# Kernel optimization log

Hardware: AMD Instinct MI355X
Metric: run time of the kernel (lower is better)

The kernel has to match this reference:

```python
import jax, jax.numpy as jnp
import numpy as np

N, L, D, A, K = 8192, 200, 64, 5, 4

def setup_inputs() -> dict:
    key = jax.random.key(0)
    k1, k2, k3, k4, k5, k6 = jax.random.split(key, 6)
    return {
        "behavior_embs": jax.random.normal(k1, (N, L, D), dtype=jnp.float32),
        "pratical_seq_len": jax.random.randint(k2, (N,), 1, L + 1),
        "W1_w": jax.random.normal(k3, (A, D), dtype=jnp.float32) * (1.0 / np.sqrt(D)),
        "W1_b": jax.random.normal(k4, (A,), dtype=jnp.float32) * 0.01,
        "W2_w": jax.random.normal(k5, (K, A), dtype=jnp.float32) * (1.0 / np.sqrt(A)),
        "W2_b": jax.random.normal(k6, (K,), dtype=jnp.float32) * 0.01,
    }

def reference(behavior_embs, pratical_seq_len, W1_w, W1_b, W2_w, W2_b):
    n, l, d = behavior_embs.shape
    valid = jnp.arange(l) < pratical_seq_len[:, None]          # [N, L] bool
    h = behavior_embs
    # tiny MLP attention scores: [N, L, K]
    s = jnp.tanh(jnp.einsum('nld,ad->nla', h, W1_w) + W1_b)
    s = jnp.einsum('nla,ka->nlk', s, W2_w) + W2_b
    s = jnp.where(valid[:, :, None], s, -jnp.inf)              # mask invalid positions
    s = jnp.swapaxes(s, -1, -2)                                # [N, K, L]
    # global-max-shifted softmax over seq dim (matches torch: subtract tensor-wide max)
    e = jnp.exp(s - jnp.max(s))                                # masked -> exp(-inf)=0
    denom = jnp.sum(e, axis=-1, keepdims=True)
    p = e / jnp.where(denom == 0, 1.0, denom)                  # all-masked rows -> 0 (torch nan->0)
    # weighted sum over sequence: [N, K, D]
    return jnp.einsum('nkl,nld->nkd', p, h)
```

## Files before the change

kernel.cpp:

```cpp
#include <hip/hip_runtime.h>
#include <math.h>


#define LL 200
#define DD 64
#define AA 5
#define KK 4
#define RPW 50
#define WU2 832
#define FREG (WU2 * 2)

__device__ __forceinline__ unsigned bf16_rne(float f) {
    unsigned u = __float_as_uint(f);
    return (u + 0x7FFFu + ((u >> 16) & 1u)) >> 16;
}
__device__ __forceinline__ unsigned pk2(float lo, float hi) {
    return bf16_rne(lo) | (bf16_rne(hi) << 16);
}
__device__ __forceinline__ float lo16(unsigned u) { return __uint_as_float(u << 16); }
__device__ __forceinline__ float hi16(unsigned u) { return __uint_as_float(u & 0xFFFF0000u); }

__device__ __forceinline__ float fast_tanh(float x) {
    float e = __expf(2.f * x);
    return 1.f - 2.f * __builtin_amdgcn_rcpf(e + 1.f);
}

__global__ __launch_bounds__(256, 5)
void mie_fused(const float* __restrict__ h_g,
               const int*   __restrict__ slen_g,
               const float* __restrict__ W1w,
               const float* __restrict__ W1b,
               const float* __restrict__ W2w,
               const float* __restrict__ W2b,
               float*       __restrict__ out)
{
    __shared__ uint2  hbuf[4 * WU2];
    __shared__ float4 p4s[4][52];
    __shared__ float  den_s[4][4][KK];

    const int n    = blockIdx.x;
    const int t    = threadIdx.x;
    const int w    = t >> 6;
    const int lane = t & 63;
    const int slen = slen_g[n];

    const int nrows = min(max(slen - w * RPW, 0), RPW);
    uint2* hbw     = &hbuf[w * WU2];
    float* fregion = (float*)hbw;

    if (nrows == 0) {
        float4 z = {0.f, 0.f, 0.f, 0.f};
        #pragma unroll
        for (int q = 0; q < 4; ++q)
            *(float4*)&fregion[q * 256 + lane * 4] = z;
        if (lane < 4) *(float4*)&den_s[w][lane][0] = z;
    } else {
        const int nf4  = slen * 16;
        const float4* hn4 = (const float4*)(h_g + (size_t)n * (LL * DD));
        const int base = w * RPW * 16;
        const int jmax = (nrows + 3) >> 2;

        for (int j0 = 0; j0 < jmax; j0 += 4) {
            float4 rn[4];
            #pragma unroll
            for (int u = 0; u < 4; ++u) {
                int i = (j0 + u) * 64 + lane;
                rn[u] = hn4[min(base + i, nf4 - 1)];
            }
            #pragma unroll
            for (int u = 0; u < 4; ++u) {
                int j = j0 + u;
                if (j < jmax) {
                    int i = j * 64 + lane;
                    int r = i >> 4, c = i & 15;
                    hbw[r * 16 + (c ^ (r & 15))] =
                        make_uint2(pk2(rn[u].x, rn[u].y), pk2(rn[u].z, rn[u].w));
                }
            }
        }

        float Bk[KK];
        #pragma unroll
        for (int k = 0; k < KK; ++k) {
            float b = fabsf(W2b[k]);
            #pragma unroll
            for (int a = 0; a < AA; ++a) b += fabsf(W2w[k * AA + a]);
            Bk[k] = b;
        }

        asm volatile("s_waitcnt lgkmcnt(0)" ::: "memory");

        const float4* W14 = (const float4*)W1w;
        const int rl = min(lane, nrows - 1);
        float a0 = W1b[0], a1 = W1b[1], a2 = W1b[2], a3 = W1b[3], a4 = W1b[4];
        #pragma unroll
        for (int i = 0; i < 16; ++i) {
            uint2 q = hbw[rl * 16 + (i ^ (rl & 15))];
            float hx = lo16(q.x), hy = hi16(q.x), hz = lo16(q.y), hw = hi16(q.y);
            float4 w0 = W14[0*16+i], w1 = W14[1*16+i], w2 = W14[2*16+i],
                   w3 = W14[3*16+i], w4 = W14[4*16+i];
            a0 = fmaf(hx, w0.x, fmaf(hy, w0.y, fmaf(hz, w0.z, fmaf(hw, w0.w, a0))));
            a1 = fmaf(hx, w1.x, fmaf(hy, w1.y, fmaf(hz, w1.z, fmaf(hw, w1.w, a1))));
            a2 = fmaf(hx, w2.x, fmaf(hy, w2.y, fmaf(hz, w2.z, fmaf(hw, w2.w, a2))));
            a3 = fmaf(hx, w3.x, fmaf(hy, w3.y, fmaf(hz, w3.z, fmaf(hw, w3.w, a3))));
            a4 = fmaf(hx, w4.x, fmaf(hy, w4.y, fmaf(hz, w4.z, fmaf(hw, w4.w, a4))));
        }
        const bool vrow = lane < nrows;
        const float t0 = fast_tanh(a0), t1 = fast_tanh(a1), t2 = fast_tanh(a2),
                    t3 = fast_tanh(a3), t4 = fast_tanh(a4);
        float e[KK];
        #pragma unroll
        for (int k = 0; k < KK; ++k) {
            float s = W2b[k];
            s = fmaf(t0, W2w[k*AA+0], s);
            s = fmaf(t1, W2w[k*AA+1], s);
            s = fmaf(t2, W2w[k*AA+2], s);
            s = fmaf(t3, W2w[k*AA+3], s);
            s = fmaf(t4, W2w[k*AA+4], s);
            e[k] = vrow ? __expf(s - Bk[k]) : 0.f;
        }
        if (lane < 52)
            p4s[w][lane] = make_float4(e[0], e[1], e[2], e[3]);

        asm volatile("s_waitcnt lgkmcnt(0)" ::: "memory");

        const int rq = lane >> 4, dc = lane & 15;
        float4 acc0 = {0,0,0,0}, acc1 = {0,0,0,0}, acc2 = {0,0,0,0}, acc3 = {0,0,0,0};
        float dn0 = 0.f, dn1 = 0.f, dn2 = 0.f, dn3 = 0.f;
        for (int g = 0; g < jmax; ++g) {
            const int row = g * 4 + rq;
            uint2 q = hbw[row * 16 + (dc ^ (row & 15))];
            float hx = lo16(q.x), hy = hi16(q.x), hz = lo16(q.y), hw = hi16(q.y);
            float4 pv = p4s[w][row];
            acc0.x = fmaf(pv.x, hx, acc0.x); acc0.y = fmaf(pv.x, hy, acc0.y);
            acc0.z = fmaf(pv.x, hz, acc0.z); acc0.w = fmaf(pv.x, hw, acc0.w);
            acc1.x = fmaf(pv.y, hx, acc1.x); acc1.y = fmaf(pv.y, hy, acc1.y);
            acc1.z = fmaf(pv.y, hz, acc1.z); acc1.w = fmaf(pv.y, hw, acc1.w);
            acc2.x = fmaf(pv.z, hx, acc2.x); acc2.y = fmaf(pv.z, hy, acc2.y);
            acc2.z = fmaf(pv.z, hz, acc2.z); acc2.w = fmaf(pv.z, hw, acc2.w);
            acc3.x = fmaf(pv.w, hx, acc3.x); acc3.y = fmaf(pv.w, hy, acc3.y);
            acc3.z = fmaf(pv.w, hz, acc3.z); acc3.w = fmaf(pv.w, hw, acc3.w);
            dn0 += pv.x; dn1 += pv.y; dn2 += pv.z; dn3 += pv.w;
        }

        *(float4*)&fregion[rq * 256 + 0 * 64 + dc * 4] = acc0;
        *(float4*)&fregion[rq * 256 + 1 * 64 + dc * 4] = acc1;
        *(float4*)&fregion[rq * 256 + 2 * 64 + dc * 4] = acc2;
        *(float4*)&fregion[rq * 256 + 3 * 64 + dc * 4] = acc3;
        if (dc == 0)
            *(float4*)&den_s[w][rq][0] = make_float4(dn0, dn1, dn2, dn3);
    }

    __syncthreads();

    {
        const float* fb = (const float*)hbuf;
        float s = 0.f;
        #pragma unroll
        for (int i = 0; i < 16; ++i)
            s += fb[(i >> 2) * FREG + (i & 3) * 256 + t];
        const int k = t >> 6;
        float den = 0.f;
        #pragma unroll
        for (int i = 0; i < 16; ++i)
            den += den_s[i >> 2][i & 3][k];
        out[(size_t)n * (KK * DD) + t] = s / den;
    }
}

extern "C" void kernel_launch(void* const* d_in, const int* in_sizes, int n_in,
                              void* d_out, int out_size, void* d_ws, size_t ws_size,
                              hipStream_t stream) {
    const float* h_g  = (const float*)d_in[0];
    const int*   slen = (const int*)  d_in[1];
    const float* W1w  = (const float*)d_in[2];
    const float* W1b  = (const float*)d_in[3];
    const float* W2w  = (const float*)d_in[4];
    const float* W2b  = (const float*)d_in[5];
    float*       outp = (float*)d_out;

    const int N = in_sizes[1];

    mie_fused<<<dim3(N), dim3(256), 0, stream>>>(h_g, slen, W1w, W1b, W2w, W2b, outp);
}
```

Measured before the change: 58.84 us.

## Convert to persistent blocks with atomic work queue and register prefetch

Replaces the one-block-per-row launch with a persistent grid of up to 1024 blocks that take rows from an atomic counter. Each wave prefetches the next row's 13 float4s per lane into registers while it computes on the current row held in LDS. The goal is to overlap global loads with compute and cut per-block launch and tail overhead. In exchange it adds a memset before every launch, an atomic per row, larger register use (occupancy hint lowered from 5 to 4), and relies on the workspace counter.

```diff
diff --git a/kernel.cpp b/kernel.cpp
--- a/kernel.cpp
+++ b/kernel.cpp
@@ -25,146 +25,177 @@
     return 1.f - 2.f * __builtin_amdgcn_rcpf(e + 1.f);
 }
 
-__global__ __launch_bounds__(256, 5)
+__global__ __launch_bounds__(256, 4)
 void mie_fused(const float* __restrict__ h_g,
                const int*   __restrict__ slen_g,
                const float* __restrict__ W1w,
                const float* __restrict__ W1b,
                const float* __restrict__ W2w,
                const float* __restrict__ W2b,
-               float*       __restrict__ out)
+               float*       __restrict__ out,
+               int*         __restrict__ ctr,
+               int N)
 {
     __shared__ uint2  hbuf[4 * WU2];
     __shared__ float4 p4s[4][52];
     __shared__ float  den_s[4][4][KK];
-
-    const int n    = blockIdx.x;
+    __shared__ int    nxt_s;
+
     const int t    = threadIdx.x;
     const int w    = t >> 6;
     const int lane = t & 63;
-    const int slen = slen_g[n];
-
-    const int nrows = min(max(slen - w * RPW, 0), RPW);
     uint2* hbw     = &hbuf[w * WU2];
     float* fregion = (float*)hbw;
-
-    if (nrows == 0) {
-        float4 z = {0.f, 0.f, 0.f, 0.f};
+    const float4* W14 = (const float4*)W1w;
+    const int base = w * RPW * 16;
+    const int G    = gridDim.x;
+
+    float Bk[KK];
+    #pragma unroll
+    for (int k = 0; k < KK; ++k) {
+        float b = fabsf(W2b[k]);
         #pragma unroll
-        for (int q = 0; q < 4; ++q)
-            *(float4*)&fregion[q * 256 + lane * 4] = z;
-        if (lane < 4) *(float4*)&den_s[w][lane][0] = z;
-    } else {
-        const int nf4  = slen * 16;
-        const float4* hn4 = (const float4*)(h_g + (size_t)n * (LL * DD));
-        const int base = w * RPW * 16;
+        for (int a = 0; a < AA; ++a) b += fabsf(W2w[k * AA + a]);
+        Bk[k] = b;
+    }
+
+    int n     = blockIdx.x;
+    int slen  = slen_g[n];
+    int nrows = min(max(slen - w * RPW, 0), RPW);
+    float4 rn[13];
+    if (nrows > 0) {
+        const float4* hp = (const float4*)(h_g + (size_t)n * (LL * DD));
+        const int nf4 = slen * 16;
+        #pragma unroll
+        for (int j = 0; j < 13; ++j)
+            rn[j] = hp[min(base + j * 64 + lane, nf4 - 1)];
+    }
+    if (t == 0) nxt_s = G + atomicAdd(ctr, 1);
+    asm volatile("s_waitcnt lgkmcnt(0)" ::: "memory");
+    __builtin_amdgcn_s_barrier();
+    int nn = __builtin_amdgcn_readfirstlane(nxt_s);
+
+    while (true) {
         const int jmax = (nrows + 3) >> 2;
 
-        for (int j0 = 0; j0 < jmax; j0 += 4) {
-            float4 rn[4];
-            #pragma unroll
-            for (int u = 0; u < 4; ++u) {
-                int i = (j0 + u) * 64 + lane;
-                rn[u] = hn4[min(base + i, nf4 - 1)];
-            }
-            #pragma unroll
-            for (int u = 0; u < 4; ++u) {
-                int j = j0 + u;
+        if (nrows == 0) {
+            float4 z = {0.f, 0.f, 0.f, 0.f};
+            #pragma unroll
+            for (int q = 0; q < 4; ++q)
+                *(float4*)&fregion[q * 256 + lane * 4] = z;
+            if (lane < 4) *(float4*)&den_s[w][lane][0] = z;
+        } else {
+            #pragma unroll
+            for (int j = 0; j < 13; ++j)
                 if (j < jmax) {
                     int i = j * 64 + lane;
                     int r = i >> 4, c = i & 15;
                     hbw[r * 16 + (c ^ (r & 15))] =
-                        make_uint2(pk2(rn[u].x, rn[u].y), pk2(rn[u].z, rn[u].w));
+                        make_uint2(pk2(rn[j].x, rn[j].y), pk2(rn[j].z, rn[j].w));
                 }
-            }
-        }
-
-        float Bk[KK];
-        #pragma unroll
-        for (int k = 0; k < KK; ++k) {
-            float b = fabsf(W2b[k]);
-            #pragma unroll
-            for (int a = 0; a < AA; ++a) b += fabsf(W2w[k * AA + a]);
-            Bk[k] = b;
+        }
+
+        int slen_n = 0, nrows_n = 0;
+        if (nn < N) {
+            slen_n  = slen_g[nn];
+            nrows_n = min(max(slen_n - w * RPW, 0), RPW);
+            if (nrows_n > 0) {
+                const float4* hp = (const float4*)(h_g + (size_t)nn * (LL * DD));
+                const int nf4 = slen_n * 16;
+                #pragma unroll
+                for (int j = 0; j < 13; ++j)
+                    rn[j] = hp[min(base + j * 64 + lane, nf4 - 1)];
+            }
+        }
+        if (t == 0) nxt_s = G + atomicAdd(ctr, 1);
+
+        if (nrows > 0) {
+            asm volatile("s_waitcnt lgkmcnt(0)" ::: "memory");
+
+            const int rl = min(lane, nrows - 1);
+            float a0 = W1b[0], a1 = W1b[1], a2 = W1b[2], a3 = W1b[3], a4 = W1b[4];
+            #pragma unroll
+            for (int i = 0; i < 16; ++i) {
+                uint2 q = hbw[rl * 16 + (i ^ (rl & 15))];
+                float hx = lo16(q.x), hy = hi16(q.x), hz = lo16(q.y), hw = hi16(q.y);
+                float4 w0 = W14[0*16+i], w1 = W14[1*16+i], w2 = W14[2*16+i],
+                       w3 = W14[3*16+i], w4 = W14[4*16+i];
+                a0 = fmaf(hx, w0.x, fmaf(hy, w0.y, fmaf(hz, w0.z, fmaf(hw, w0.w, a0))));
+                a1 = fmaf(hx, w1.x, fmaf(hy, w1.y, fmaf(hz, w1.z, fmaf(hw, w1.w, a1))));
+                a2 = fmaf(hx, w2.x, fmaf(hy, w2.y, fmaf(hz, w2.z, fmaf(hw, w2.w, a2))));
+                a3 = fmaf(hx, w3.x, fmaf(hy, w3.y, fmaf(hz, w3.z, fmaf(hw, w3.w, a3))));
+                a4 = fmaf(hx, w4.x, fmaf(hy, w4.y, fmaf(hz, w4.z, fmaf(hw, w4.w, a4))));
+            }
+            const bool vrow = lane < nrows;
+            const float t0 = fast_tanh(a0), t1 = fast_tanh(a1), t2 = fast_tanh(a2),
+                        t3 = fast_tanh(a3), t4 = fast_tanh(a4);
+            float e[KK];
+            #pragma unroll
+            for (int k = 0; k < KK; ++k) {
+                float s = W2b[k];
+                s = fmaf(t0, W2w[k*AA+0], s);
+                s = fmaf(t1, W2w[k*AA+1], s);
+                s = fmaf(t2, W2w[k*AA+2], s);
+                s = fmaf(t3, W2w[k*AA+3], s);
+                s = fmaf(t4, W2w[k*AA+4], s);
+                e[k] = vrow ? __expf(s - Bk[k]) : 0.f;
+            }
+            if (lane < 52)
+                p4s[w][lane] = make_float4(e[0], e[1], e[2], e[3]);
+
+            asm volatile("s_waitcnt lgkmcnt(0)" ::: "memory");
+
+            const int rq = lane >> 4, dc = lane & 15;
+            float4 acc0 = {0,0,0,0}, acc1 = {0,0,0,0},
+                   acc2 = {0,0,0,0}, acc3 = {0,0,0,0};
+            float dn0 = 0.f, dn1 = 0.f, dn2 = 0.f, dn3 = 0.f;
+            for (int g = 0; g < jmax; ++g) {
+                const int row = g * 4 + rq;
+                uint2 q = hbw[row * 16 + (dc ^ (row & 15))];
+                float hx = lo16(q.x), hy = hi16(q.x), hz = lo16(q.y), hw = hi16(q.y);
+                float4 pv = p4s[w][row];
+                acc0.x = fmaf(pv.x, hx, acc0.x); acc0.y = fmaf(pv.x, hy, acc0.y);
+                acc0.z = fmaf(pv.x, hz, acc0.z); acc0.w = fmaf(pv.x, hw, acc0.w);
+                acc1.x = fmaf(pv.y, hx, acc1.x); acc1.y = fmaf(pv.y, hy, acc1.y);
+                acc1.z = fmaf(pv.y, hz, acc1.z); acc1.w = fmaf(pv.y, hw, acc1.w);
+                acc2.x = fmaf(pv.z, hx, acc2.x); acc2.y = fmaf(pv.z, hy, acc2.y);
+                acc2.z = fmaf(pv.z, hz, acc2.z); acc2.w = fmaf(pv.z, hw, acc2.w);
+                acc3.x = fmaf(pv.w, hx, acc3.x); acc3.y = fmaf(pv.w, hy, acc3.y);
+                acc3.z = fmaf(pv.w, hz, acc3.z); acc3.w = fmaf(pv.w, hw, acc3.w);
+                dn0 += pv.x; dn1 += pv.y; dn2 += pv.z; dn3 += pv.w;
+            }
+
+            *(float4*)&fregion[rq * 256 + 0 * 64 + dc * 4] = acc0;
+            *(float4*)&fregion[rq * 256 + 1 * 64 + dc * 4] = acc1;
+            *(float4*)&fregion[rq * 256 + 2 * 64 + dc * 4] = acc2;
+            *(float4*)&fregion[rq * 256 + 3 * 64 + dc * 4] = acc3;
+            if (dc == 0)
+                *(float4*)&den_s[w][rq][0] = make_float4(dn0, dn1, dn2, dn3);
         }
 
         asm volatile("s_waitcnt lgkmcnt(0)" ::: "memory");
-
-        const float4* W14 = (const float4*)W1w;
-        const int rl = min(lane, nrows - 1);
-        float a0 = W1b[0], a1 = W1b[1], a2 = W1b[2], a3 = W1b[3], a4 = W1b[4];
-        #pragma unroll
-        for (int i = 0; i < 16; ++i) {
-            uint2 q = hbw[rl * 16 + (i ^ (rl & 15))];
-            float hx = lo16(q.x), hy = hi16(q.x), hz = lo16(q.y), hw = hi16(q.y);
-            float4 w0 = W14[0*16+i], w1 = W14[1*16+i], w2 = W14[2*16+i],
-                   w3 = W14[3*16+i], w4 = W14[4*16+i];
-            a0 = fmaf(hx, w0.x, fmaf(hy, w0.y, fmaf(hz, w0.z, fmaf(hw, w0.w, a0))));
-            a1 = fmaf(hx, w1.x, fmaf(hy, w1.y, fmaf(hz, w1.z, fmaf(hw, w1.w, a1))));
-            a2 = fmaf(hx, w2.x, fmaf(hy, w2.y, fmaf(hz, w2.z, fmaf(hw, w2.w, a2))));
-            a3 = fmaf(hx, w3.x, fmaf(hy, w3.y, fmaf(hz, w3.z, fmaf(hw, w3.w, a3))));
-            a4 = fmaf(hx, w4.x, fmaf(hy, w4.y, fmaf(hz, w4.z, fmaf(hw, w4.w, a4))));
-        }
-        const bool vrow = lane < nrows;
-        const float t0 = fast_tanh(a0), t1 = fast_tanh(a1), t2 = fast_tanh(a2),
-                    t3 = fast_tanh(a3), t4 = fast_tanh(a4);
-        float e[KK];
-        #pragma unroll
-        for (int k = 0; k < KK; ++k) {
-            float s = W2b[k];
-            s = fmaf(t0, W2w[k*AA+0], s);
-            s = fmaf(t1, W2w[k*AA+1], s);
-            s = fmaf(t2, W2w[k*AA+2], s);
-            s = fmaf(t3, W2w[k*AA+3], s);
-            s = fmaf(t4, W2w[k*AA+4], s);
-            e[k] = vrow ? __expf(s - Bk[k]) : 0.f;
-        }
-        if (lane < 52)
-            p4s[w][lane] = make_float4(e[0], e[1], e[2], e[3]);
+        __builtin_amdgcn_s_barrier();
+
+        {
+            const float* fb = (const float*)hbuf;
+            float s = 0.f;
+            #pragma unroll
+            for (int i = 0; i < 16; ++i)
+                s += fb[(i >> 2) * FREG + (i & 3) * 256 + t];
+            const int k = t >> 6;
+            float den = 0.f;
+            #pragma unroll
+            for (int i = 0; i < 16; ++i)
+                den += den_s[i >> 2][i & 3][k];
+            out[(size_t)n * (KK * DD) + t] = s / den;
+        }
+        const int nn2 = __builtin_amdgcn_readfirstlane(nxt_s);
 
         asm volatile("s_waitcnt lgkmcnt(0)" ::: "memory");
-
-        const int rq = lane >> 4, dc = lane & 15;
-        float4 acc0 = {0,0,0,0}, acc1 = {0,0,0,0}, acc2 = {0,0,0,0}, acc3 = {0,0,0,0};
-        float dn0 = 0.f, dn1 = 0.f, dn2 = 0.f, dn3 = 0.f;
-        for (int g = 0; g < jmax; ++g) {
-            const int row = g * 4 + rq;
-            uint2 q = hbw[row * 16 + (dc ^ (row & 15))];
-            float hx = lo16(q.x), hy = hi16(q.x), hz = lo16(q.y), hw = hi16(q.y);
-            float4 pv = p4s[w][row];
-            acc0.x = fmaf(pv.x, hx, acc0.x); acc0.y = fmaf(pv.x, hy, acc0.y);
-            acc0.z = fmaf(pv.x, hz, acc0.z); acc0.w = fmaf(pv.x, hw, acc0.w);
-            acc1.x = fmaf(pv.y, hx, acc1.x); acc1.y = fmaf(pv.y, hy, acc1.y);
-            acc1.z = fmaf(pv.y, hz, acc1.z); acc1.w = fmaf(pv.y, hw, acc1.w);
-            acc2.x = fmaf(pv.z, hx, acc2.x); acc2.y = fmaf(pv.z, hy, acc2.y);
-            acc2.z = fmaf(pv.z, hz, acc2.z); acc2.w = fmaf(pv.z, hw, acc2.w);
-            acc3.x = fmaf(pv.w, hx, acc3.x); acc3.y = fmaf(pv.w, hy, acc3.y);
-            acc3.z = fmaf(pv.w, hz, acc3.z); acc3.w = fmaf(pv.w, hw, acc3.w);
-            dn0 += pv.x; dn1 += pv.y; dn2 += pv.z; dn3 += pv.w;
-        }
-
-        *(float4*)&fregion[rq * 256 + 0 * 64 + dc * 4] = acc0;
-        *(float4*)&fregion[rq * 256 + 1 * 64 + dc * 4] = acc1;
-        *(float4*)&fregion[rq * 256 + 2 * 64 + dc * 4] = acc2;
-        *(float4*)&fregion[rq * 256 + 3 * 64 + dc * 4] = acc3;
-        if (dc == 0)
-            *(float4*)&den_s[w][rq][0] = make_float4(dn0, dn1, dn2, dn3);
-    }
-
-    __syncthreads();
-
-    {
-        const float* fb = (const float*)hbuf;
-        float s = 0.f;
-        #pragma unroll
-        for (int i = 0; i < 16; ++i)
-            s += fb[(i >> 2) * FREG + (i & 3) * 256 + t];
-        const int k = t >> 6;
-        float den = 0.f;
-        #pragma unroll
-        for (int i = 0; i < 16; ++i)
-            den += den_s[i >> 2][i & 3][k];
-        out[(size_t)n * (KK * DD) + t] = s / den;
+        __builtin_amdgcn_s_barrier();
+
+        n = nn; slen = slen_n; nrows = nrows_n; nn = nn2;
+        if (n >= N) break;
     }
 }
 
@@ -178,8 +209,12 @@
     const float* W2w  = (const float*)d_in[4];
     const float* W2b  = (const float*)d_in[5];
     float*       outp = (float*)d_out;
+    int*         ctr  = (int*)d_ws;
 
     const int N = in_sizes[1];
-
-    mie_fused<<<dim3(N), dim3(256), 0, stream>>>(h_g, slen, W1w, W1b, W2w, W2b, outp);
-}
+    const int grid = (N < 1024) ? N : 1024;
+
+    hipMemsetAsync(d_ws, 0, sizeof(int), stream);
+    mie_fused<<<dim3(grid), dim3(256), 0, stream>>>(h_g, slen, W1w, W1b, W2w,
+                                                    W2b, outp, ctr, N);
+}
```

Result: slower. 130.3 us (+121.4%).
